# Optimization experiments

Hardware: AMD Instinct MI355X
Metric: run time of the kernel (lower is better)

The kernel has to match this reference:

```python
import jax, jax.numpy as jnp
import numpy as np
from jax import lax

K_NEIGHBORS = 3  # n_neighbors


def _divide_no_nan(x, d):
    # tf.math.divide_no_nan semantics: 0 where denominator is 0
    safe = jnp.where(d == 0, 1.0, d)
    return jnp.where(d == 0, 0.0, x / safe)


def setup_inputs() -> dict:
    key = jax.random.key(0)
    k1, k2, k3 = jax.random.split(key, 3)
    B, N, D, C = 512, 200000, 27, 10
    queries = jax.random.normal(k1, (B, D), dtype=jnp.float32)
    features = jax.random.normal(k2, (N, D), dtype=jnp.float32)
    cls = jax.random.randint(k3, (N,), 0, C)
    labels = jax.nn.one_hot(cls, C, dtype=jnp.float32)
    return {"queries": queries, "features": features, "labels": labels}


def reference(queries, features, labels):
    # scale_tensor: per-dim max of |training features| (computed at init in the TF model)
    scale = jnp.max(jnp.abs(features), axis=0)              # (D,)
    fs = _divide_no_nan(features, scale)                    # (N, D)
    qs = _divide_no_nan(queries, scale)                     # (B, D)

    # pairwise Euclidean distances (B, N) == tf.norm(fs - q, axis=1) per query
    d2 = (jnp.sum(fs * fs, axis=1)[None, :]
          - 2.0 * qs @ fs.T
          + jnp.sum(qs * qs, axis=1)[:, None])
    dist = jnp.sqrt(jnp.maximum(d2, 0.0))                   # (B, N)

    neg_kd, idx = lax.top_k(-dist, K_NEIGHBORS)             # (B, K)
    kd = -neg_kd                                            # k smallest distances
    lab = labels[idx]                                       # (B, K, C) gather

    # weighted vote: sum_k label_k / dist_k, then argmax -> one-hot
    safe_kd = jnp.where(kd == 0, 1.0, kd)
    weighted = jnp.sum(lab / safe_kd[..., None], axis=1)    # (B, C)
    vote = jax.nn.one_hot(jnp.argmax(weighted, axis=-1), labels.shape[1],
                          dtype=labels.dtype)

    # exact-match branch: if min distance == 0, take nearest neighbor's label
    zero_hit = (jnp.min(kd, axis=1, keepdims=True) == 0)    # (B, 1)
    result = jnp.where(zero_hit, lab[:, 0, :], vote)        # (B, C)

    # concatenated (k_smallest_distances, result_tensor) per query: (B, K + C)
    return jnp.concatenate([kd, result], axis=-1)
```

## Files before the change

kernel.cpp:

```cpp
#include <hip/hip_runtime.h>
#include <math.h>

#define NQ   512
#define DD   27
#define NC   10
#define KK   3
#define FC   128
#define FCD  (FC*DD)
#define NTHR 256

static __device__ __forceinline__ unsigned fbits(float x){ return __float_as_uint(x); }

__global__ void k_scale(const float* __restrict__ feats, unsigned* __restrict__ scale_bits,
                        int total, int total_f4) {
  __shared__ unsigned smax[DD];
  int t = threadIdx.x;
  if (t < DD) smax[t] = 0u;
  __syncthreads();
  int gid = blockIdx.x * blockDim.x + t;
  int stride = gridDim.x * blockDim.x;
  const float4* f4 = (const float4*)feats;
  float m0=0.f, m1=0.f, m2=0.f, m3=0.f;
  for (int i = gid; i < total_f4; i += stride) {
    float4 v = f4[i];
    m0 = fmaxf(m0, fabsf(v.x));
    m1 = fmaxf(m1, fabsf(v.y));
    m2 = fmaxf(m2, fabsf(v.z));
    m3 = fmaxf(m3, fabsf(v.w));
  }
  int d0 = (4*gid) % DD;
  atomicMax(&smax[d0],          fbits(m0));
  atomicMax(&smax[(d0+1)%DD],   fbits(m1));
  atomicMax(&smax[(d0+2)%DD],   fbits(m2));
  atomicMax(&smax[(d0+3)%DD],   fbits(m3));
  if (gid == 0) {
    for (int i = total_f4*4; i < total; ++i)
      atomicMax(&scale_bits[i % DD], fbits(fabsf(feats[i])));
  }
  __syncthreads();
  if (t < DD) atomicMax(&scale_bits[t], smax[t]);
}

__global__ void k_prep(const float* __restrict__ queries, const unsigned* __restrict__ scale_bits,
                       float* __restrict__ rscale, float* __restrict__ qs,
                       float* __restrict__ qnorm) {
  __shared__ float rs[DD];
  int t = threadIdx.x;
  if (t < DD) {
    float s = __uint_as_float(scale_bits[t]);
    float r = (s == 0.f) ? 0.f : 1.f / s;
    rs[t] = r;
    rscale[t] = r;
  }
  __syncthreads();
  float nrm = 0.f;
  #pragma unroll
  for (int d = 0; d < DD; ++d) {
    float v = queries[t*DD + d] * rs[d];
    qs[t*DD + d] = v;
    nrm = fmaf(v, v, nrm);
  }
  qnorm[t] = nrm;
}

__global__ __launch_bounds__(NTHR) void k_knn(
    const float* __restrict__ feats, const float* __restrict__ rscale,
    const float* __restrict__ qs, float* __restrict__ pd2, int* __restrict__ pidx,
    int nchunks, int nblk, int nfeat) {
  __shared__ float lds[FC*28];
  int t = threadIdx.x;
  float q0[28], q1[28];
  #pragma unroll
  for (int d = 0; d < DD; ++d) {
    q0[d] = qs[t*DD + d];
    q1[d] = qs[(t+NTHR)*DD + d];
  }
  q0[27] = -0.5f; q1[27] = -0.5f;
  float s00=-INFINITY, s01=-INFINITY, s02=-INFINITY;
  float s10=-INFINITY, s11=-INFINITY, s12=-INFINITY;
  int   i00=0x7fffffff, i01=0x7fffffff, i02=0x7fffffff;
  int   i10=0x7fffffff, i11=0x7fffffff, i12=0x7fffffff;
  int ntot = nfeat * DD;

  for (int c = blockIdx.x; c < nchunks; c += nblk) {
    __syncthreads();
    int base = c * FCD;
    #pragma unroll
    for (int j = 0; j < 14; ++j) {
      int i = t + j*NTHR;
      if (i < FCD) {
        int f = i / DD;
        int d = i - f*DD;
        int gi = base + i;
        float v = (gi < ntot) ? feats[gi] * rscale[d] : 0.f;
        lds[f*28 + d] = v;
      }
    }
    __syncthreads();
    if (t < FC) {
      float sm = 0.f;
      #pragma unroll
      for (int d = 0; d < DD; ++d) { float v = lds[t*28 + d]; sm = fmaf(v, v, sm); }
      int fg = c*FC + t;
      lds[t*28 + 27] = (fg < nfeat) ? sm : INFINITY;
    }
    __syncthreads();
    const float4* lf = (const float4*)lds;
    #pragma unroll 2
    for (int f = 0; f < FC; ++f) {
      float a0a=0.f, a0b=0.f, a1a=0.f, a1b=0.f;
      #pragma unroll
      for (int j = 0; j < 7; ++j) {
        float4 v = lf[f*7 + j];
        if ((j & 1) == 0) {
          a0a = fmaf(v.x, q0[4*j+0], a0a);
          a0a = fmaf(v.y, q0[4*j+1], a0a);
          a0a = fmaf(v.z, q0[4*j+2], a0a);
          a0a = fmaf(v.w, q0[4*j+3], a0a);
          a1a = fmaf(v.x, q1[4*j+0], a1a);
          a1a = fmaf(v.y, q1[4*j+1], a1a);
          a1a = fmaf(v.z, q1[4*j+2], a1a);
          a1a = fmaf(v.w, q1[4*j+3], a1a);
        } else {
          a0b = fmaf(v.x, q0[4*j+0], a0b);
          a0b = fmaf(v.y, q0[4*j+1], a0b);
          a0b = fmaf(v.z, q0[4*j+2], a0b);
          a0b = fmaf(v.w, q0[4*j+3], a0b);
          a1b = fmaf(v.x, q1[4*j+0], a1b);
          a1b = fmaf(v.y, q1[4*j+1], a1b);
          a1b = fmaf(v.z, q1[4*j+2], a1b);
          a1b = fmaf(v.w, q1[4*j+3], a1b);
        }
      }
      float acc0 = a0a + a0b;
      float acc1 = a1a + a1b;
      int fi = c*FC + f;
      if (acc0 > s02) {
        if (acc0 > s00)      { s02=s01;i02=i01; s01=s00;i01=i00; s00=acc0;i00=fi; }
        else if (acc0 > s01) { s02=s01;i02=i01; s01=acc0;i01=fi; }
        else                 { s02=acc0; i02=fi; }
      }
      if (acc1 > s12) {
        if (acc1 > s10)      { s12=s11;i12=i11; s11=s10;i11=i10; s10=acc1;i10=fi; }
        else if (acc1 > s11) { s12=s11;i12=i11; s11=acc1;i11=fi; }
        else                 { s12=acc1; i12=fi; }
      }
    }
  }
  long off0 = ((long)t * nblk + blockIdx.x) * 3;
  pd2[off0+0] = -2.f*s00; pd2[off0+1] = -2.f*s01; pd2[off0+2] = -2.f*s02;
  pidx[off0+0] = i00;     pidx[off0+1] = i01;     pidx[off0+2] = i02;
  long off1 = ((long)(t+NTHR) * nblk + blockIdx.x) * 3;
  pd2[off1+0] = -2.f*s10; pd2[off1+1] = -2.f*s11; pd2[off1+2] = -2.f*s12;
  pidx[off1+0] = i10;     pidx[off1+1] = i11;     pidx[off1+2] = i12;
}

#define INS(vv, ii) do { \
  if ((vv) < c2 || ((vv) == c2 && (ii) < j2)) { \
    if ((vv) < c0 || ((vv) == c0 && (ii) < j0))      { c2=c1;j2=j1; c1=c0;j1=j0; c0=(vv);j0=(ii); } \
    else if ((vv) < c1 || ((vv) == c1 && (ii) < j1)) { c2=c1;j2=j1; c1=(vv);j1=(ii); } \
    else                                             { c2=(vv); j2=(ii); } \
  } \
} while (0)

__global__ __launch_bounds__(NTHR) void k_merge(
    const float* __restrict__ pd2, const int* __restrict__ pidx,
    const float* __restrict__ qnorm, const float* __restrict__ labels,
    float* __restrict__ out, int nblk) {
  __shared__ float sk[NTHR*3];
  __shared__ int   si[NTHR*3];
  int q = blockIdx.x, t = threadIdx.x;
  float c0=INFINITY, c1=INFINITY, c2=INFINITY;
  int   j0=0x7fffffff, j1=0x7fffffff, j2=0x7fffffff;
  int ncand = nblk * 3;
  const float* pq = pd2  + (long)q * nblk * 3;
  const int*   iq = pidx + (long)q * nblk * 3;
  for (int i = t; i < ncand; i += NTHR) {
    float v = pq[i]; int ix = iq[i];
    INS(v, ix);
  }
  sk[t*3+0]=c0; sk[t*3+1]=c1; sk[t*3+2]=c2;
  si[t*3+0]=j0; si[t*3+1]=j1; si[t*3+2]=j2;
  __syncthreads();
  if (t < 64) {
    for (int s = 1; s < 4; ++s) {
      int b = t + s*64;
      #pragma unroll
      for (int k = 0; k < 3; ++k) { float v = sk[b*3+k]; int ix = si[b*3+k]; INS(v, ix); }
    }
    sk[t*3+0]=c0; sk[t*3+1]=c1; sk[t*3+2]=c2;
    si[t*3+0]=j0; si[t*3+1]=j1; si[t*3+2]=j2;
  }
  __syncthreads();
  if (t == 0) {
    for (int s = 1; s < 64; ++s) {
      #pragma unroll
      for (int k = 0; k < 3; ++k) { float v = sk[s*3+k]; int ix = si[s*3+k]; INS(v, ix); }
    }
    float qn = qnorm[q];
    float kd0 = sqrtf(fmaxf(c0 + qn, 0.f));
    float kd1 = sqrtf(fmaxf(c1 + qn, 0.f));
    float kd2 = sqrtf(fmaxf(c2 + qn, 0.f));
    const float* l0 = labels + (long)j0 * NC;
    const float* l1 = labels + (long)j1 * NC;
    const float* l2 = labels + (long)j2 * NC;
    float inv0 = 1.f / ((kd0 == 0.f) ? 1.f : kd0);
    float inv1 = 1.f / ((kd1 == 0.f) ? 1.f : kd1);
    float inv2 = 1.f / ((kd2 == 0.f) ? 1.f : kd2);
    float w[NC];
    #pragma unroll
    for (int cc = 0; cc < NC; ++cc)
      w[cc] = l0[cc]*inv0 + l1[cc]*inv1 + l2[cc]*inv2;
    int am = 0; float bw = w[0];
    #pragma unroll
    for (int cc = 1; cc < NC; ++cc) if (w[cc] > bw) { bw = w[cc]; am = cc; }
    float* o = out + q * (KK + NC);
    o[0] = kd0; o[1] = kd1; o[2] = kd2;
    if (kd0 == 0.f) {
      #pragma unroll
      for (int cc = 0; cc < NC; ++cc) o[3+cc] = l0[cc];
    } else {
      #pragma unroll
      for (int cc = 0; cc < NC; ++cc) o[3+cc] = (cc == am) ? 1.f : 0.f;
    }
  }
}

extern "C" void kernel_launch(void* const* d_in, const int* in_sizes, int n_in,
                              void* d_out, int out_size, void* d_ws, size_t ws_size,
                              hipStream_t stream) {
  const float* queries = (const float*)d_in[0];
  const float* feats   = (const float*)d_in[1];
  const float* labels  = (const float*)d_in[2];
  float* out = (float*)d_out;
  char*  ws  = (char*)d_ws;

  int total = in_sizes[1];
  int nfeat = total / DD;
  unsigned* scale_bits = (unsigned*)ws;
  float* rscale = (float*)(ws + 128);
  float* qnorm  = (float*)(ws + 256);
  float* qs     = (float*)(ws + 2304);
  float* pd2    = (float*)(ws + 65536);

  int nchunks = (nfeat + FC - 1) / FC;
  long cap = (ws_size > 65536) ? (long)((ws_size - 65536) / ((long)NQ*3*8)) : 1;
  int nblk = (int)((cap < (long)nchunks) ? cap : (long)nchunks);
  if (nblk < 1) nblk = 1;
  int* pidx = (int*)(ws + 65536 + (long)nblk * NQ * 3 * 4);

  hipMemsetAsync(ws, 0, 128, stream);
  k_scale<<<432, 256, 0, stream>>>(feats, scale_bits, total, total / 4);
  k_prep <<<1, NQ, 0, stream>>>(queries, scale_bits, rscale, qs, qnorm);
  k_knn  <<<nblk, NTHR, 0, stream>>>(feats, rscale, qs, pd2, pidx, nchunks, nblk, nfeat);
  k_merge<<<NQ, NTHR, 0, stream>>>(pd2, pidx, qnorm, labels, out, nblk);
}
```

Before: 270.8 us.

## Restructure kNN as per-wave dynamic work queue with 4 queries per lane

The chunked LDS-staged kNN kernel is replaced by a wave-level design. Each wave holds 4 queries per lane (half of the 512 queries per wave) and pulls 32-feature tasks from an atomic counter. Feature rows are read straight from global memory as wave-uniform scalar loads, and the feature scaling is folded into the query (q*rscale^2). A separate kernel precomputes the scaled feature norms. This removes LDS staging, the block barriers and the per-chunk scaling work, at the cost of more registers per thread, an extra kernel launch and twice the total feature reads (each half re-reads all features).

```diff
diff --git a/kernel.cpp b/kernel.cpp
--- a/kernel.cpp
+++ b/kernel.cpp
@@ -5,9 +5,11 @@
 #define DD   27
 #define NC   10
 #define KK   3
-#define FC   128
-#define FCD  (FC*DD)
 #define NTHR 256
+#define TF   32
+#define KNN_BLOCKS 512
+#define NWAVE (KNN_BLOCKS*4)
+#define NWHALF (NWAVE/2)
 
 static __device__ __forceinline__ unsigned fbits(float x){ return __float_as_uint(x); }
 
@@ -42,7 +44,7 @@
 }
 
 __global__ void k_prep(const float* __restrict__ queries, const unsigned* __restrict__ scale_bits,
-                       float* __restrict__ rscale, float* __restrict__ qs,
+                       float* __restrict__ rscale, float* __restrict__ qp,
                        float* __restrict__ qnorm) {
   __shared__ float rs[DD];
   int t = threadIdx.x;
@@ -57,102 +59,94 @@
   #pragma unroll
   for (int d = 0; d < DD; ++d) {
     float v = queries[t*DD + d] * rs[d];
-    qs[t*DD + d] = v;
+    qp[t*DD + d] = v * rs[d];
     nrm = fmaf(v, v, nrm);
   }
   qnorm[t] = nrm;
 }
 
-__global__ __launch_bounds__(NTHR) void k_knn(
-    const float* __restrict__ feats, const float* __restrict__ rscale,
-    const float* __restrict__ qs, float* __restrict__ pd2, int* __restrict__ pidx,
-    int nchunks, int nblk, int nfeat) {
-  __shared__ float lds[FC*28];
-  int t = threadIdx.x;
-  float q0[28], q1[28];
-  #pragma unroll
-  for (int d = 0; d < DD; ++d) {
-    q0[d] = qs[t*DD + d];
-    q1[d] = qs[(t+NTHR)*DD + d];
-  }
-  q0[27] = -0.5f; q1[27] = -0.5f;
-  float s00=-INFINITY, s01=-INFINITY, s02=-INFINITY;
-  float s10=-INFINITY, s11=-INFINITY, s12=-INFINITY;
-  int   i00=0x7fffffff, i01=0x7fffffff, i02=0x7fffffff;
-  int   i10=0x7fffffff, i11=0x7fffffff, i12=0x7fffffff;
-  int ntot = nfeat * DD;
-
-  for (int c = blockIdx.x; c < nchunks; c += nblk) {
-    __syncthreads();
-    int base = c * FCD;
-    #pragma unroll
-    for (int j = 0; j < 14; ++j) {
-      int i = t + j*NTHR;
-      if (i < FCD) {
-        int f = i / DD;
-        int d = i - f*DD;
-        int gi = base + i;
-        float v = (gi < ntot) ? feats[gi] * rscale[d] : 0.f;
-        lds[f*28 + d] = v;
-      }
-    }
-    __syncthreads();
-    if (t < FC) {
-      float sm = 0.f;
-      #pragma unroll
-      for (int d = 0; d < DD; ++d) { float v = lds[t*28 + d]; sm = fmaf(v, v, sm); }
-      int fg = c*FC + t;
-      lds[t*28 + 27] = (fg < nfeat) ? sm : INFINITY;
-    }
-    __syncthreads();
-    const float4* lf = (const float4*)lds;
+__global__ void k_fnorm(const float* __restrict__ feats, const float* __restrict__ rscale,
+                        float* __restrict__ fnorm2, int nfeat) {
+  __shared__ float rs[DD];
+  int t = threadIdx.x;
+  if (t < DD) rs[t] = rscale[t];
+  __syncthreads();
+  int f = blockIdx.x * blockDim.x + t;
+  if (f < nfeat) {
+    const float* row = feats + f*DD;
+    float acc = 0.f;
+    #pragma unroll
+    for (int d = 0; d < DD; ++d) { float v = row[d] * rs[d]; acc = fmaf(v, v, acc); }
+    fnorm2[f] = acc;
+  }
+}
+
+#define FEAT_BODY(f) do {                                                   \
+    const float* row_ = feats + (f)*DD;                                     \
+    float fn_ = fnorm2[(f)];                                                \
+    float a_[4];                                                            \
+    _Pragma("unroll")                                                       \
+    for (int k_ = 0; k_ < 4; ++k_) a_[k_] = fn_ * -0.5f;                    \
+    _Pragma("unroll")                                                       \
+    for (int d_ = 0; d_ < DD; ++d_) {                                       \
+      float fv_ = row_[d_];         \
+      _Pragma("unroll")                                                     \
+      for (int k_ = 0; k_ < 4; ++k_) a_[k_] = fmaf(fv_, q[k_][d_], a_[k_]); \
+    }                                                                       \
+    _Pragma("unroll")                                                       \
+    for (int k_ = 0; k_ < 4; ++k_) {                                        \
+      float acc_ = a_[k_];                                                  \
+      if (acc_ > s2[k_]) {                                                  \
+        if (acc_ > s0[k_])      { s2[k_]=s1[k_];i2[k_]=i1[k_]; s1[k_]=s0[k_];i1[k_]=i0[k_]; s0[k_]=acc_;i0[k_]=(f); } \
+        else if (acc_ > s1[k_]) { s2[k_]=s1[k_];i2[k_]=i1[k_]; s1[k_]=acc_;i1[k_]=(f); } \
+        else                    { s2[k_]=acc_; i2[k_]=(f); }                \
+      }                                                                     \
+    }                                                                       \
+  } while (0)
+
+__global__ __launch_bounds__(NTHR, 2) void k_knn(
+    const float* __restrict__ feats, const float* __restrict__ qp,
+    const float* __restrict__ fnorm2, float* __restrict__ pd2,
+    int* __restrict__ pidx, unsigned* __restrict__ ctr, int ntask, int nfeat) {
+  int t = threadIdx.x;
+  int lane = t & 63;
+  int wid  = blockIdx.x * 4 + (t >> 6);
+  int half = wid & 1;
+  float q[4][DD];
+  #pragma unroll
+  for (int k = 0; k < 4; ++k) {
+    int qq = half*256 + k*64 + lane;
+    #pragma unroll
+    for (int d = 0; d < DD; ++d) q[k][d] = qp[qq*DD + d];
+  }
+  float s0[4], s1[4], s2[4];
+  int   i0[4], i1[4], i2[4];
+  #pragma unroll
+  for (int k = 0; k < 4; ++k) { s0[k]=s1[k]=s2[k]=-INFINITY; i0[k]=i1[k]=i2[k]=0x7fffffff; }
+
+  for (;;) {
+    unsigned c = 0;
+    if (lane == 0) c = atomicAdd(&ctr[half], 1u);
+    c = (unsigned)__builtin_amdgcn_readfirstlane((int)c);
+    if ((int)c >= ntask) break;
+    int f0 = (int)c * TF;
     #pragma unroll 2
-    for (int f = 0; f < FC; ++f) {
-      float a0a=0.f, a0b=0.f, a1a=0.f, a1b=0.f;
-      #pragma unroll
-      for (int j = 0; j < 7; ++j) {
-        float4 v = lf[f*7 + j];
-        if ((j & 1) == 0) {
-          a0a = fmaf(v.x, q0[4*j+0], a0a);
-          a0a = fmaf(v.y, q0[4*j+1], a0a);
-          a0a = fmaf(v.z, q0[4*j+2], a0a);
-          a0a = fmaf(v.w, q0[4*j+3], a0a);
-          a1a = fmaf(v.x, q1[4*j+0], a1a);
-          a1a = fmaf(v.y, q1[4*j+1], a1a);
-          a1a = fmaf(v.z, q1[4*j+2], a1a);
-          a1a = fmaf(v.w, q1[4*j+3], a1a);
-        } else {
-          a0b = fmaf(v.x, q0[4*j+0], a0b);
-          a0b = fmaf(v.y, q0[4*j+1], a0b);
-          a0b = fmaf(v.z, q0[4*j+2], a0b);
-          a0b = fmaf(v.w, q0[4*j+3], a0b);
-          a1b = fmaf(v.x, q1[4*j+0], a1b);
-          a1b = fmaf(v.y, q1[4*j+1], a1b);
-          a1b = fmaf(v.z, q1[4*j+2], a1b);
-          a1b = fmaf(v.w, q1[4*j+3], a1b);
-        }
-      }
-      float acc0 = a0a + a0b;
-      float acc1 = a1a + a1b;
-      int fi = c*FC + f;
-      if (acc0 > s02) {
-        if (acc0 > s00)      { s02=s01;i02=i01; s01=s00;i01=i00; s00=acc0;i00=fi; }
-        else if (acc0 > s01) { s02=s01;i02=i01; s01=acc0;i01=fi; }
-        else                 { s02=acc0; i02=fi; }
-      }
-      if (acc1 > s12) {
-        if (acc1 > s10)      { s12=s11;i12=i11; s11=s10;i11=i10; s10=acc1;i10=fi; }
-        else if (acc1 > s11) { s12=s11;i12=i11; s11=acc1;i11=fi; }
-        else                 { s12=acc1; i12=fi; }
-      }
-    }
-  }
-  long off0 = ((long)t * nblk + blockIdx.x) * 3;
-  pd2[off0+0] = -2.f*s00; pd2[off0+1] = -2.f*s01; pd2[off0+2] = -2.f*s02;
-  pidx[off0+0] = i00;     pidx[off0+1] = i01;     pidx[off0+2] = i02;
-  long off1 = ((long)(t+NTHR) * nblk + blockIdx.x) * 3;
-  pd2[off1+0] = -2.f*s10; pd2[off1+1] = -2.f*s11; pd2[off1+2] = -2.f*s12;
-  pidx[off1+0] = i10;     pidx[off1+1] = i11;     pidx[off1+2] = i12;
+    for (int ff = 0; ff < TF; ++ff) {
+      int f = f0 + ff;
+      FEAT_BODY(f);
+    }
+  }
+  int remStart = ntask * TF;
+  if (wid < 2 && remStart < nfeat) {
+    for (int f = remStart; f < nfeat; ++f) FEAT_BODY(f);
+  }
+
+  #pragma unroll
+  for (int k = 0; k < 4; ++k) {
+    int off = (wid*256 + k*64 + lane)*3;
+    pd2[off+0] = -2.f*s0[k]; pd2[off+1] = -2.f*s1[k]; pd2[off+2] = -2.f*s2[k];
+    pidx[off+0] = i0[k];     pidx[off+1] = i1[k];     pidx[off+2] = i2[k];
+  }
 }
 
 #define INS(vv, ii) do { \
@@ -166,18 +160,18 @@
 __global__ __launch_bounds__(NTHR) void k_merge(
     const float* __restrict__ pd2, const int* __restrict__ pidx,
     const float* __restrict__ qnorm, const float* __restrict__ labels,
-    float* __restrict__ out, int nblk) {
+    float* __restrict__ out) {
   __shared__ float sk[NTHR*3];
   __shared__ int   si[NTHR*3];
   int q = blockIdx.x, t = threadIdx.x;
+  int half = q >> 8, qs_ = q & 255;
   float c0=INFINITY, c1=INFINITY, c2=INFINITY;
   int   j0=0x7fffffff, j1=0x7fffffff, j2=0x7fffffff;
-  int ncand = nblk * 3;
-  const float* pq = pd2  + (long)q * nblk * 3;
-  const int*   iq = pidx + (long)q * nblk * 3;
-  for (int i = t; i < ncand; i += NTHR) {
-    float v = pq[i]; int ix = iq[i];
-    INS(v, ix);
+  for (int w = t; w < NWHALF; w += NTHR) {
+    int wid = 2*w + half;
+    int base = (wid*256 + qs_)*3;
+    #pragma unroll
+    for (int j = 0; j < 3; ++j) { float v = pd2[base+j]; int ix = pidx[base+j]; INS(v, ix); }
   }
   sk[t*3+0]=c0; sk[t*3+1]=c1; sk[t*3+2]=c2;
   si[t*3+0]=j0; si[t*3+1]=j1; si[t*3+2]=j2;
@@ -237,21 +231,22 @@
 
   int total = in_sizes[1];
   int nfeat = total / DD;
-  unsigned* scale_bits = (unsigned*)ws;
-  float* rscale = (float*)(ws + 128);
-  float* qnorm  = (float*)(ws + 256);
-  float* qs     = (float*)(ws + 2304);
-  float* pd2    = (float*)(ws + 65536);
-
-  int nchunks = (nfeat + FC - 1) / FC;
-  long cap = (ws_size > 65536) ? (long)((ws_size - 65536) / ((long)NQ*3*8)) : 1;
-  int nblk = (int)((cap < (long)nchunks) ? cap : (long)nchunks);
-  if (nblk < 1) nblk = 1;
-  int* pidx = (int*)(ws + 65536 + (long)nblk * NQ * 3 * 4);
-
-  hipMemsetAsync(ws, 0, 128, stream);
+
+  unsigned* ctr        = (unsigned*)ws;
+  unsigned* scale_bits = (unsigned*)(ws + 64);
+  float* rscale = (float*)(ws + 256);
+  float* qnorm  = (float*)(ws + 512);
+  float* qp     = (float*)(ws + 4096);
+  float* fnorm2 = (float*)(ws + 65536);
+  float* pd2    = (float*)(ws + 1048576);
+  int*   pidx   = (int*)(ws + 8388608);
+
+  int ntask = nfeat / TF;
+
+  hipMemsetAsync(ws, 0, 256, stream);
   k_scale<<<432, 256, 0, stream>>>(feats, scale_bits, total, total / 4);
-  k_prep <<<1, NQ, 0, stream>>>(queries, scale_bits, rscale, qs, qnorm);
-  k_knn  <<<nblk, NTHR, 0, stream>>>(feats, rscale, qs, pd2, pidx, nchunks, nblk, nfeat);
-  k_merge<<<NQ, NTHR, 0, stream>>>(pd2, pidx, qnorm, labels, out, nblk);
-}
+  k_prep <<<1, NQ, 0, stream>>>(queries, scale_bits, rscale, qp, qnorm);
+  k_fnorm<<<(nfeat + 255) / 256, 256, 0, stream>>>(feats, rscale, fnorm2, nfeat);
+  k_knn  <<<KNN_BLOCKS, NTHR, 0, stream>>>(feats, qp, fnorm2, pd2, pidx, ctr, ntask, nfeat);
+  k_merge<<<NQ, NTHR, 0, stream>>>(pd2, pidx, qnorm, labels, out);
+}
```

Measured after the change: 366.1 us. +35.2%, slower.
